# Performance work log

Measured on AMD Instinct MI355X. Metric: run time of the kernel, lower is better.

Reference implementation:

```python
import jax, jax.numpy as jnp
import numpy as np

BC, N, F, D = 16, 2048, 128, 128
N_EDGES = 65536
NEG_INF = -1e16
LEAK = 0.1


def setup_inputs() -> dict:
    key = jax.random.key(0)
    k_h, k_w, k_r, k_c = jax.random.split(key, 4)
    h = jax.random.normal(k_h, (BC, N, F), dtype=jnp.float32)
    # xavier_normal with gain 1.414
    w_std = 1.414 * np.sqrt(2.0 / (F + D))
    W = jax.random.normal(k_w, (F, D), dtype=jnp.float32) * w_std
    row = jax.random.randint(k_r, (N_EDGES,), 0, N, dtype=jnp.int64)
    col = jax.random.randint(k_c, (N_EDGES,), 0, N, dtype=jnp.int64)
    return {"h": h, "W": W, "row": row, "col": col}


def reference(h, W, row, col):
    bc, n, f = h.shape
    # z = h @ W : [bc, N, D]
    z = jnp.einsum("bnf,fd->bnd", h, W)
    # dense inner-product attention scores [bc, N, N]
    att = jnp.einsum("bnd,bmd->bnm", z, z)
    # leaky_relu(0.1)
    att = jnp.where(att > 0, att, LEAK * att)
    # sparse adjacency mask built from COO indices
    mask = jnp.zeros((n, n), dtype=att.dtype).at[row, col].set(1.0)
    att = att * mask[None, :, :]
    # masked_fill where value == 0 (non-edges, and incidental exact zeros)
    att = jnp.where(att == 0.0, NEG_INF, att)
    att = jax.nn.softmax(att, axis=2)
    # aggregate: [bc, N, N] @ [bc, N, D]
    return jnp.einsum("bnm,bmd->bnd", att, z)
```

## Files before the change

### kernel.cpp

```cpp
#include <hip/hip_runtime.h>

#define BC 16
#define NN 2048
#define FF 128
#define DD 128
#define NEDGES 65536
#define NEG_INF -1e16f
#define LEAK 0.1f
#define CAPR 128
#define THRS 20.0f

typedef __attribute__((ext_vector_type(8))) short s16x8;
typedef __attribute__((ext_vector_type(4))) float f32x4;

__device__ __forceinline__ unsigned short f2bf(float x) {
    const unsigned int u = __float_as_uint(x);
    return (unsigned short)((u + 0x7FFFu + ((u >> 16) & 1u)) >> 16);
}
__device__ __forceinline__ float bf2f(unsigned short b) {
    return __uint_as_float(((unsigned int)b) << 16);
}

__global__ void __launch_bounds__(256) wprep_kernel(const float* __restrict__ W,
                                                    unsigned short* __restrict__ Wp) {
    const int idx = blockIdx.x * 256 + threadIdx.x;
    const float4 v = ((const float4*)W)[idx];
    const int k = idx >> 5;
    const int d0 = (idx & 31) << 2;
    const int kb = k * 2;
    const int base = kb & ~15, within = kb & 15;
    const float vv[4] = {v.x, v.y, v.z, v.w};
#pragma unroll
    for (int c = 0; c < 4; ++c) {
        const int d = d0 + c;
        const unsigned short hi = f2bf(vv[c]);
        const unsigned short lo = f2bf(vv[c] - bf2f(hi));
        const int off = d * 512 + ((base ^ ((d & 7) << 4)) | within);
        Wp[off >> 1] = hi;
        Wp[(off + 256) >> 1] = lo;
    }
}

__global__ void __launch_bounds__(256) zedge_kernel(const float* __restrict__ h,
                                                    const unsigned short* __restrict__ Wp,
                                                    float* __restrict__ z,
                                                    const int* __restrict__ row,
                                                    const int* __restrict__ col,
                                                    unsigned int* __restrict__ mask) {
    __shared__ unsigned short Wb[FF * DD * 2];
    const int tid = threadIdx.x;
    const int blk = blockIdx.x;

    if (blk < 256) {
        const int e = blk * 256 + tid;
        const unsigned int key = (unsigned int)row[e] * NN + (unsigned int)col[e];
        atomicOr(&mask[key >> 5], 1u << (key & 31u));
        return;
    }

    {
        const float4* wg = (const float4*)Wp;
        float4* wl = (float4*)Wb;
#pragma unroll
        for (int i = 0; i < 16; ++i) wl[tid + 256 * i] = wg[tid + 256 * i];
    }
    __syncthreads();

    const int ln = tid & 63, wv = tid >> 6;
    const int m0 = (blk - 256) * 64 + wv * 16;
    const int mr = m0 + (ln & 15);
    const int koct = (ln >> 4) * 8;

    s16x8 ah[4], al[4];
#pragma unroll
    for (int k0 = 0; k0 < 4; ++k0) {
        const float* hp = h + (size_t)mr * FF + k0 * 32 + koct;
        const float4 p = *(const float4*)hp;
        const float4 q = *(const float4*)(hp + 4);
        const float x[8] = {p.x, p.y, p.z, p.w, q.x, q.y, q.z, q.w};
        s16x8 hi8, lo8;
#pragma unroll
        for (int i = 0; i < 8; ++i) {
            const unsigned short hb = f2bf(x[i]);
            hi8[i] = (short)hb;
            lo8[i] = (short)f2bf(x[i] - bf2f(hb));
        }
        ah[k0] = hi8; al[k0] = lo8;
    }

    f32x4 acc[8] = {};
#pragma unroll
    for (int k0 = 0; k0 < 4; ++k0) {
#pragma unroll
        for (int dt = 0; dt < 8; ++dt) {
            const int d = dt * 16 + (ln & 15);
            const int kb = (k0 * 32 + koct) * 2;
            const int off = d * 512 + (kb ^ ((d & 7) << 4));
            const s16x8 bh = *(const s16x8*)((const char*)Wb + off);
            const s16x8 bl = *(const s16x8*)((const char*)Wb + off + 256);
            acc[dt] = __builtin_amdgcn_mfma_f32_16x16x32_bf16(ah[k0], bh, acc[dt], 0, 0, 0);
            acc[dt] = __builtin_amdgcn_mfma_f32_16x16x32_bf16(al[k0], bh, acc[dt], 0, 0, 0);
            acc[dt] = __builtin_amdgcn_mfma_f32_16x16x32_bf16(ah[k0], bl, acc[dt], 0, 0, 0);
        }
    }

    const int dcol = ln & 15;
    const int rbase = m0 + (ln >> 4) * 4;
#pragma unroll
    for (int dt = 0; dt < 8; ++dt)
#pragma unroll
        for (int r = 0; r < 4; ++r)
            z[(size_t)(rbase + r) * DD + dt * 16 + dcol] = acc[dt][r];
}

__global__ void __launch_bounds__(256) gat_kernel(const float* __restrict__ z,
                                                  const unsigned int* __restrict__ mask,
                                                  float* __restrict__ out) {
    __shared__ unsigned short hits_l[4][CAPR];
    const int tid = threadIdx.x, wv = tid >> 6, ln = tid & 63;
    const int blk = blockIdx.x;
    const int b = ((blk & 7) << 1) | (wv & 1);
    const int n = ((blk >> 3) << 1) | (wv >> 1);
    const int eq = ln >> 3, hq = ln & 7;

    unsigned int bits = mask[n * 64 + ln];
    const int cnt = __popc(bits);
    int pre = cnt;
#pragma unroll
    for (int off = 1; off <= 32; off <<= 1) {
        const int t = __shfl_up(pre, off, 64);
        if (ln >= off) pre += t;
    }
    const int total = __shfl(pre, 63, 64);
    int slot = pre - cnt;
    while (bits) {
        const int bit = __ffs(bits) - 1;
        bits &= bits - 1;
        if (slot < CAPR) hits_l[wv][slot] = (unsigned short)(ln * 32 + bit);
        ++slot;
    }
    const int nh = min(total, CAPR);
    const int hv0 = hits_l[wv][ln];
    const int hv1 = hits_l[wv][64 + ln];

    const float* zb = z + ((size_t)b << 18);
    const float4* znp = (const float4*)(zb + ((size_t)n << 7) + (hq << 4));
    const float4 a0 = znp[0], a1 = znp[1], a2 = znp[2], a3 = znp[3];

    float m = NEG_INF, l = 0.f;
    float4 acc0 = make_float4(0.f, 0.f, 0.f, 0.f), acc1 = acc0, acc2 = acc0, acc3 = acc0;

#pragma unroll 2
    for (int c0 = 0; c0 < nh; c0 += 8) {
        const int e = c0 + eq;
        const int hv = (c0 < 64) ? hv0 : hv1;
        const int he = __shfl(hv, e & 63, 64) & (NN - 1);
        const float4* zc = (const float4*)(zb + ((size_t)he << 7) + (hq << 4));
        const float4 v0 = zc[0], v1 = zc[1], v2 = zc[2], v3 = zc[3];
        float ch0 = a0.x * v0.x + a0.y * v0.y + a0.z * v0.z + a0.w * v0.w
                  + a1.x * v1.x + a1.y * v1.y + a1.z * v1.z + a1.w * v1.w;
        float ch1 = a2.x * v2.x + a2.y * v2.y + a2.z * v2.z + a2.w * v2.w
                  + a3.x * v3.x + a3.y * v3.y + a3.z * v3.z + a3.w * v3.w;
        float pt = ch0 + ch1;
        pt += __shfl_xor(pt, 1, 64);
        pt += __shfl_xor(pt, 2, 64);
        pt += __shfl_xor(pt, 4, 64);
        float sv = pt > 0.f ? pt : LEAK * pt;
        if (sv == 0.f || e >= nh) sv = NEG_INF;

        if (__any(sv - m > THRS)) {
            const float mnew = fmaxf(m, sv);
            const float alpha = __expf(m - mnew);
            m = mnew;
            l *= alpha;
            acc0.x *= alpha; acc0.y *= alpha; acc0.z *= alpha; acc0.w *= alpha;
            acc1.x *= alpha; acc1.y *= alpha; acc1.z *= alpha; acc1.w *= alpha;
            acc2.x *= alpha; acc2.y *= alpha; acc2.z *= alpha; acc2.w *= alpha;
            acc3.x *= alpha; acc3.y *= alpha; acc3.z *= alpha; acc3.w *= alpha;
        }
        const float pr = __expf(sv - m);
        l += pr;
        acc0.x += pr * v0.x; acc0.y += pr * v0.y; acc0.z += pr * v0.z; acc0.w += pr * v0.w;
        acc1.x += pr * v1.x; acc1.y += pr * v1.y; acc1.z += pr * v1.z; acc1.w += pr * v1.w;
        acc2.x += pr * v2.x; acc2.y += pr * v2.y; acc2.z += pr * v2.z; acc2.w += pr * v2.w;
        acc3.x += pr * v3.x; acc3.y += pr * v3.y; acc3.z += pr * v3.z; acc3.w += pr * v3.w;
    }

    float M = m;
#pragma unroll
    for (int off = 8; off <= 32; off <<= 1) M = fmaxf(M, __shfl_xor(M, off, 64));

    if (nh > 0 && M > 0.5f * NEG_INF) {
        const float al = __expf(m - M);
        l *= al;
        acc0.x *= al; acc0.y *= al; acc0.z *= al; acc0.w *= al;
        acc1.x *= al; acc1.y *= al; acc1.z *= al; acc1.w *= al;
        acc2.x *= al; acc2.y *= al; acc2.z *= al; acc2.w *= al;
        acc3.x *= al; acc3.y *= al; acc3.z *= al; acc3.w *= al;
#pragma unroll
        for (int off = 8; off <= 32; off <<= 1) {
            l += __shfl_xor(l, off, 64);
            acc0.x += __shfl_xor(acc0.x, off, 64); acc0.y += __shfl_xor(acc0.y, off, 64);
            acc0.z += __shfl_xor(acc0.z, off, 64); acc0.w += __shfl_xor(acc0.w, off, 64);
            acc1.x += __shfl_xor(acc1.x, off, 64); acc1.y += __shfl_xor(acc1.y, off, 64);
            acc1.z += __shfl_xor(acc1.z, off, 64); acc1.w += __shfl_xor(acc1.w, off, 64);
            acc2.x += __shfl_xor(acc2.x, off, 64); acc2.y += __shfl_xor(acc2.y, off, 64);
            acc2.z += __shfl_xor(acc2.z, off, 64); acc2.w += __shfl_xor(acc2.w, off, 64);
            acc3.x += __shfl_xor(acc3.x, off, 64); acc3.y += __shfl_xor(acc3.y, off, 64);
            acc3.z += __shfl_xor(acc3.z, off, 64); acc3.w += __shfl_xor(acc3.w, off, 64);
        }
        const float inv = 1.f / l;
        acc0.x *= inv; acc0.y *= inv; acc0.z *= inv; acc0.w *= inv;
        acc1.x *= inv; acc1.y *= inv; acc1.z *= inv; acc1.w *= inv;
        acc2.x *= inv; acc2.y *= inv; acc2.z *= inv; acc2.w *= inv;
        acc3.x *= inv; acc3.y *= inv; acc3.z *= inv; acc3.w *= inv;
    } else {
        acc0 = make_float4(0.f, 0.f, 0.f, 0.f); acc1 = acc0; acc2 = acc0; acc3 = acc0;
        for (int mm = 0; mm < NN; ++mm) {
            const float4* zr = (const float4*)(zb + ((size_t)mm << 7) + (hq << 4));
            const float4 t0 = zr[0], t1 = zr[1], t2 = zr[2], t3 = zr[3];
            acc0.x += t0.x; acc0.y += t0.y; acc0.z += t0.z; acc0.w += t0.w;
            acc1.x += t1.x; acc1.y += t1.y; acc1.z += t1.z; acc1.w += t1.w;
            acc2.x += t2.x; acc2.y += t2.y; acc2.z += t2.z; acc2.w += t2.w;
            acc3.x += t3.x; acc3.y += t3.y; acc3.z += t3.z; acc3.w += t3.w;
        }
        const float s = 1.f / NN;
        acc0.x *= s; acc0.y *= s; acc0.z *= s; acc0.w *= s;
        acc1.x *= s; acc1.y *= s; acc1.z *= s; acc1.w *= s;
        acc2.x *= s; acc2.y *= s; acc2.z *= s; acc2.w *= s;
        acc3.x *= s; acc3.y *= s; acc3.z *= s; acc3.w *= s;
    }

    if (eq < 4) {
        float4 o = acc0;
        if (eq == 1) o = acc1;
        if (eq == 2) o = acc2;
        if (eq == 3) o = acc3;
        *(float4*)(out + (((size_t)b * NN + n) << 7) + (hq << 4) + (eq << 2)) = o;
    }
}

extern "C" void kernel_launch(void* const* d_in, const int* in_sizes, int n_in,
                              void* d_out, int out_size, void* d_ws, size_t ws_size,
                              hipStream_t stream) {
    const float* h = (const float*)d_in[0];
    const float* W = (const float*)d_in[1];
    const int* row = (const int*)d_in[2];
    const int* col = (const int*)d_in[3];
    float* out = (float*)d_out;

    char* ws = (char*)d_ws;
    float* z = (float*)ws;
    unsigned int* mask = (unsigned int*)(ws + (size_t)16 * 1024 * 1024);
    unsigned short* Wp = (unsigned short*)(ws + (size_t)16 * 1024 * 1024 + 512 * 1024);

    hipMemsetAsync(mask, 0, (size_t)NN * NN / 8, stream);
    wprep_kernel<<<16, 256, 0, stream>>>(W, Wp);
    zedge_kernel<<<768, 256, 0, stream>>>(h, Wp, z, row, col, mask);
    gat_kernel<<<(BC * NN) / 4, 256, 0, stream>>>(z, mask, out);
}
```

Baseline: 136.3 us.

## Fold mask clearing into wprep kernel and read W fragments directly from global

Drops the separate hipMemsetAsync by having extra wprep blocks zero the adjacency bitmask. The z projection kernel no longer stages the 64KB split-bf16 W in LDS with a barrier; each wave loads its B fragments straight from global/L2 in a plain [d][k] layout, and launch bounds now request 3 blocks per SM. This removes the LDS copy and sync and raises occupancy, but replaces LDS reads with repeated global loads that depend on cache hits.

```diff
diff --git a/kernel.cpp b/kernel.cpp
--- a/kernel.cpp
+++ b/kernel.cpp
@@ -22,32 +22,39 @@
 }
 
 __global__ void __launch_bounds__(256) wprep_kernel(const float* __restrict__ W,
-                                                    unsigned short* __restrict__ Wp) {
-    const int idx = blockIdx.x * 256 + threadIdx.x;
+                                                    unsigned short* __restrict__ Wp,
+                                                    unsigned int* __restrict__ mask) {
+    const int blk = blockIdx.x, tid = threadIdx.x;
+    if (blk >= 16) {
+        uint4* mv = (uint4*)mask;
+        const int t0 = (blk - 16) * 256 + tid;
+#pragma unroll
+        for (int j = 0; j < 3; ++j) {
+            const int i = t0 + j * 12288;
+            if (i < NN * NN / 128) mv[i] = make_uint4(0u, 0u, 0u, 0u);
+        }
+        return;
+    }
+    const int idx = blk * 256 + tid;
     const float4 v = ((const float4*)W)[idx];
     const int k = idx >> 5;
     const int d0 = (idx & 31) << 2;
-    const int kb = k * 2;
-    const int base = kb & ~15, within = kb & 15;
     const float vv[4] = {v.x, v.y, v.z, v.w};
 #pragma unroll
     for (int c = 0; c < 4; ++c) {
         const int d = d0 + c;
         const unsigned short hi = f2bf(vv[c]);
-        const unsigned short lo = f2bf(vv[c] - bf2f(hi));
-        const int off = d * 512 + ((base ^ ((d & 7) << 4)) | within);
-        Wp[off >> 1] = hi;
-        Wp[(off + 256) >> 1] = lo;
-    }
-}
-
-__global__ void __launch_bounds__(256) zedge_kernel(const float* __restrict__ h,
-                                                    const unsigned short* __restrict__ Wp,
-                                                    float* __restrict__ z,
-                                                    const int* __restrict__ row,
-                                                    const int* __restrict__ col,
-                                                    unsigned int* __restrict__ mask) {
-    __shared__ unsigned short Wb[FF * DD * 2];
+        Wp[d * 128 + k] = hi;
+        Wp[16384 + d * 128 + k] = f2bf(vv[c] - bf2f(hi));
+    }
+}
+
+__global__ void __launch_bounds__(256, 3) zedge_kernel(const float* __restrict__ h,
+                                                       const unsigned short* __restrict__ Wp,
+                                                       float* __restrict__ z,
+                                                       const int* __restrict__ row,
+                                                       const int* __restrict__ col,
+                                                       unsigned int* __restrict__ mask) {
     const int tid = threadIdx.x;
     const int blk = blockIdx.x;
 
@@ -57,14 +64,6 @@
         atomicOr(&mask[key >> 5], 1u << (key & 31u));
         return;
     }
-
-    {
-        const float4* wg = (const float4*)Wp;
-        float4* wl = (float4*)Wb;
-#pragma unroll
-        for (int i = 0; i < 16; ++i) wl[tid + 256 * i] = wg[tid + 256 * i];
-    }
-    __syncthreads();
 
     const int ln = tid & 63, wv = tid >> 6;
     const int m0 = (blk - 256) * 64 + wv * 16;
@@ -88,29 +87,32 @@
         ah[k0] = hi8; al[k0] = lo8;
     }
 
+    const int dlane = ln & 15;
     f32x4 acc[8] = {};
 #pragma unroll
     for (int k0 = 0; k0 < 4; ++k0) {
+        const int kbase = k0 * 32 + koct;
+        s16x8 bh[8], bl[8];
 #pragma unroll
         for (int dt = 0; dt < 8; ++dt) {
-            const int d = dt * 16 + (ln & 15);
-            const int kb = (k0 * 32 + koct) * 2;
-            const int off = d * 512 + (kb ^ ((d & 7) << 4));
-            const s16x8 bh = *(const s16x8*)((const char*)Wb + off);
-            const s16x8 bl = *(const s16x8*)((const char*)Wb + off + 256);
-            acc[dt] = __builtin_amdgcn_mfma_f32_16x16x32_bf16(ah[k0], bh, acc[dt], 0, 0, 0);
-            acc[dt] = __builtin_amdgcn_mfma_f32_16x16x32_bf16(al[k0], bh, acc[dt], 0, 0, 0);
-            acc[dt] = __builtin_amdgcn_mfma_f32_16x16x32_bf16(ah[k0], bl, acc[dt], 0, 0, 0);
-        }
-    }
-
-    const int dcol = ln & 15;
+            const int d = dt * 16 + dlane;
+            bh[dt] = *(const s16x8*)(Wp + d * 128 + kbase);
+            bl[dt] = *(const s16x8*)(Wp + 16384 + d * 128 + kbase);
+        }
+#pragma unroll
+        for (int dt = 0; dt < 8; ++dt) {
+            acc[dt] = __builtin_amdgcn_mfma_f32_16x16x32_bf16(ah[k0], bh[dt], acc[dt], 0, 0, 0);
+            acc[dt] = __builtin_amdgcn_mfma_f32_16x16x32_bf16(al[k0], bh[dt], acc[dt], 0, 0, 0);
+            acc[dt] = __builtin_amdgcn_mfma_f32_16x16x32_bf16(ah[k0], bl[dt], acc[dt], 0, 0, 0);
+        }
+    }
+
     const int rbase = m0 + (ln >> 4) * 4;
 #pragma unroll
     for (int dt = 0; dt < 8; ++dt)
 #pragma unroll
         for (int r = 0; r < 4; ++r)
-            z[(size_t)(rbase + r) * DD + dt * 16 + dcol] = acc[dt][r];
+            z[(size_t)(rbase + r) * DD + dt * 16 + dlane] = acc[dt][r];
 }
 
 __global__ void __launch_bounds__(256) gat_kernel(const float* __restrict__ z,
@@ -252,10 +254,9 @@
     char* ws = (char*)d_ws;
     float* z = (float*)ws;
     unsigned int* mask = (unsigned int*)(ws + (size_t)16 * 1024 * 1024);
-    unsigned short* Wp = (unsigned short*)(ws + (size_t)16 * 1024 * 1024 + 512 * 1024);
-
-    hipMemsetAsync(mask, 0, (size_t)NN * NN / 8, stream);
-    wprep_kernel<<<16, 256, 0, stream>>>(W, Wp);
+    unsigned short* Wp = (unsigned short*)(ws + (size_t)17 * 1024 * 1024 + 512 * 1024);
+
+    wprep_kernel<<<64, 256, 0, stream>>>(W, Wp, mask);
     zedge_kernel<<<768, 256, 0, stream>>>(h, Wp, z, row, col, mask);
     gat_kernel<<<(BC * NN) / 4, 256, 0, stream>>>(z, mask, out);
 }
```

Result: slower. 144.9 us (+6.3%).

## Fold mask memset into wprep kernel, double rows per zedge block, unroll gat loop

Applied to the files above, without the earlier changes.

Drops the separate hipMemsetAsync and clears the adjacency bitmask inside extra blocks of the W-prep kernel, removing one launch. The projection kernel now has each wave compute two 16-row tiles, so 256 projection blocks replace 512 and the LDS copy of W is amortized over twice the rows. The attention loop unroll goes from 2 to 4 to expose more gather loads in flight. The costs are higher register pressure in both kernels and fewer blocks for the projection.

```diff
diff --git a/kernel.cpp b/kernel.cpp
--- a/kernel.cpp
+++ b/kernel.cpp
@@ -22,8 +22,20 @@
 }
 
 __global__ void __launch_bounds__(256) wprep_kernel(const float* __restrict__ W,
-                                                    unsigned short* __restrict__ Wp) {
-    const int idx = blockIdx.x * 256 + threadIdx.x;
+                                                    unsigned short* __restrict__ Wp,
+                                                    unsigned int* __restrict__ mask) {
+    const int blk = blockIdx.x, tid = threadIdx.x;
+    if (blk >= 16) {
+        uint4* mv = (uint4*)mask;
+        const int t0 = (blk - 16) * 256 + tid;
+#pragma unroll
+        for (int j = 0; j < 3; ++j) {
+            const int i = t0 + j * 12288;
+            if (i < NN * NN / 128) mv[i] = make_uint4(0u, 0u, 0u, 0u);
+        }
+        return;
+    }
+    const int idx = blk * 256 + tid;
     const float4 v = ((const float4*)W)[idx];
     const int k = idx >> 5;
     const int d0 = (idx & 31) << 2;
@@ -67,50 +79,54 @@
     __syncthreads();
 
     const int ln = tid & 63, wv = tid >> 6;
-    const int m0 = (blk - 256) * 64 + wv * 16;
-    const int mr = m0 + (ln & 15);
     const int koct = (ln >> 4) * 8;
-
-    s16x8 ah[4], al[4];
-#pragma unroll
-    for (int k0 = 0; k0 < 4; ++k0) {
-        const float* hp = h + (size_t)mr * FF + k0 * 32 + koct;
-        const float4 p = *(const float4*)hp;
-        const float4 q = *(const float4*)(hp + 4);
-        const float x[8] = {p.x, p.y, p.z, p.w, q.x, q.y, q.z, q.w};
-        s16x8 hi8, lo8;
-#pragma unroll
-        for (int i = 0; i < 8; ++i) {
-            const unsigned short hb = f2bf(x[i]);
-            hi8[i] = (short)hb;
-            lo8[i] = (short)f2bf(x[i] - bf2f(hb));
-        }
-        ah[k0] = hi8; al[k0] = lo8;
-    }
-
-    f32x4 acc[8] = {};
-#pragma unroll
-    for (int k0 = 0; k0 < 4; ++k0) {
-#pragma unroll
-        for (int dt = 0; dt < 8; ++dt) {
-            const int d = dt * 16 + (ln & 15);
-            const int kb = (k0 * 32 + koct) * 2;
-            const int off = d * 512 + (kb ^ ((d & 7) << 4));
-            const s16x8 bh = *(const s16x8*)((const char*)Wb + off);
-            const s16x8 bl = *(const s16x8*)((const char*)Wb + off + 256);
-            acc[dt] = __builtin_amdgcn_mfma_f32_16x16x32_bf16(ah[k0], bh, acc[dt], 0, 0, 0);
-            acc[dt] = __builtin_amdgcn_mfma_f32_16x16x32_bf16(al[k0], bh, acc[dt], 0, 0, 0);
-            acc[dt] = __builtin_amdgcn_mfma_f32_16x16x32_bf16(ah[k0], bl, acc[dt], 0, 0, 0);
-        }
-    }
-
-    const int dcol = ln & 15;
-    const int rbase = m0 + (ln >> 4) * 4;
-#pragma unroll
-    for (int dt = 0; dt < 8; ++dt)
-#pragma unroll
-        for (int r = 0; r < 4; ++r)
-            z[(size_t)(rbase + r) * DD + dt * 16 + dcol] = acc[dt][r];
+    const int dlane = ln & 15;
+
+#pragma unroll
+    for (int mt = 0; mt < 2; ++mt) {
+        const int m0 = (blk - 256) * 128 + wv * 32 + mt * 16;
+        const int mr = m0 + (ln & 15);
+
+        s16x8 ah[4], al[4];
+#pragma unroll
+        for (int k0 = 0; k0 < 4; ++k0) {
+            const float* hp = h + (size_t)mr * FF + k0 * 32 + koct;
+            const float4 p = *(const float4*)hp;
+            const float4 q = *(const float4*)(hp + 4);
+            const float x[8] = {p.x, p.y, p.z, p.w, q.x, q.y, q.z, q.w};
+            s16x8 hi8, lo8;
+#pragma unroll
+            for (int i = 0; i < 8; ++i) {
+                const unsigned short hb = f2bf(x[i]);
+                hi8[i] = (short)hb;
+                lo8[i] = (short)f2bf(x[i] - bf2f(hb));
+            }
+            ah[k0] = hi8; al[k0] = lo8;
+        }
+
+        f32x4 acc[8] = {};
+#pragma unroll
+        for (int k0 = 0; k0 < 4; ++k0) {
+#pragma unroll
+            for (int dt = 0; dt < 8; ++dt) {
+                const int d = dt * 16 + dlane;
+                const int kb = (k0 * 32 + koct) * 2;
+                const int off = d * 512 + (kb ^ ((d & 7) << 4));
+                const s16x8 bh = *(const s16x8*)((const char*)Wb + off);
+                const s16x8 bl = *(const s16x8*)((const char*)Wb + off + 256);
+                acc[dt] = __builtin_amdgcn_mfma_f32_16x16x32_bf16(ah[k0], bh, acc[dt], 0, 0, 0);
+                acc[dt] = __builtin_amdgcn_mfma_f32_16x16x32_bf16(al[k0], bh, acc[dt], 0, 0, 0);
+                acc[dt] = __builtin_amdgcn_mfma_f32_16x16x32_bf16(ah[k0], bl, acc[dt], 0, 0, 0);
+            }
+        }
+
+        const int rbase = m0 + (ln >> 4) * 4;
+#pragma unroll
+        for (int dt = 0; dt < 8; ++dt)
+#pragma unroll
+            for (int r = 0; r < 4; ++r)
+                z[(size_t)(rbase + r) * DD + dt * 16 + dlane] = acc[dt][r];
+    }
 }
 
 __global__ void __launch_bounds__(256) gat_kernel(const float* __restrict__ z,
@@ -150,7 +166,7 @@
     float m = NEG_INF, l = 0.f;
     float4 acc0 = make_float4(0.f, 0.f, 0.f, 0.f), acc1 = acc0, acc2 = acc0, acc3 = acc0;
 
-#pragma unroll 2
+#pragma unroll 4
     for (int c0 = 0; c0 < nh; c0 += 8) {
         const int e = c0 + eq;
         const int hv = (c0 < 64) ? hv0 : hv1;
@@ -252,10 +268,9 @@
     char* ws = (char*)d_ws;
     float* z = (float*)ws;
     unsigned int* mask = (unsigned int*)(ws + (size_t)16 * 1024 * 1024);
-    unsigned short* Wp = (unsigned short*)(ws + (size_t)16 * 1024 * 1024 + 512 * 1024);
-
-    hipMemsetAsync(mask, 0, (size_t)NN * NN / 8, stream);
-    wprep_kernel<<<16, 256, 0, stream>>>(W, Wp);
-    zedge_kernel<<<768, 256, 0, stream>>>(h, Wp, z, row, col, mask);
+    unsigned short* Wp = (unsigned short*)(ws + (size_t)17 * 1024 * 1024 + 512 * 1024);
+
+    wprep_kernel<<<64, 256, 0, stream>>>(W, Wp, mask);
+    zedge_kernel<<<512, 256, 0, stream>>>(h, Wp, z, row, col, mask);
     gat_kernel<<<(BC * NN) / 4, 256, 0, stream>>>(z, mask, out);
 }
```

After: 135.4 us. No clear change (-0.6%).
